# Kernel optimization log

Measured on AMD Instinct MI355X. Metric: run time of the kernel, lower is better.

Reference implementation:

```python
import jax, jax.numpy as jnp
import numpy as np

S, B, H = 2048, 4, 1024

def setup_inputs() -> dict:
    key = jax.random.key(0)
    ks = jax.random.split(key, 9)
    s = 1.0 / np.sqrt(H)
    return {
        "x": jax.random.normal(ks[0], (S, B, H), jnp.float32),
        "ssm": jax.random.normal(ks[1], (B, S, S), jnp.float32),
        "Wq": jax.random.uniform(ks[2], (H, H), jnp.float32, -s, s),
        "bq": jax.random.uniform(ks[3], (H,), jnp.float32, -s, s),
        "Wk": jax.random.uniform(ks[4], (H, H), jnp.float32, -s, s),
        "bk": jax.random.uniform(ks[5], (H,), jnp.float32, -s, s),
        "Wv": jax.random.uniform(ks[6], (H, H), jnp.float32, -s, s),
        "bv": jax.random.uniform(ks[7], (H,), jnp.float32, -s, s),
        "beta": jnp.array(1.0, jnp.float32),
    }

def reference(x, ssm, Wq, bq, Wk, bk, Wv, bv, beta):
    scale = x.shape[-1] ** 0.5
    # projections on [S,B,H], then move to [B,S,H]
    Q = jnp.einsum('sbh,oh->bso', x, Wq) + bq
    K = jnp.einsum('sbh,oh->bso', x, Wk) + bk
    V = jnp.einsum('sbh,oh->bso', x, Wv) + bv
    scores = jnp.einsum('bqh,bkh->bqk', Q, K) / scale + beta * ssm
    attn = jax.nn.softmax(scores, axis=-1)
    out = jnp.einsum('bqk,bkh->bqh', attn, V)  # [B,S,H]
    return out.transpose(1, 0, 2)  # [S,B,H]
```

## Files before the change

kernel.cpp:

```cpp
#include <hip/hip_runtime.h>
#include <stdint.h>


#define S_LEN 2048
#define BATCH 4
#define HDIM  1024

typedef unsigned short u16;
typedef float f32x4  __attribute__((ext_vector_type(4)));
typedef short bf16x8 __attribute__((ext_vector_type(8)));
typedef u16   u16x4  __attribute__((ext_vector_type(4)));

#define AS1 __attribute__((address_space(1)))
#define AS3 __attribute__((address_space(3)))

__device__ __forceinline__ u16 f2bf(float f) {
  union { float f; uint32_t u; } c; c.f = f;
  uint32_t u = c.u;
  u += 0x7fffu + ((u >> 16) & 1u);
  return (u16)(u >> 16);
}

__global__ __launch_bounds__(256)
void cast_all(const float* __restrict__ x,
              const float* __restrict__ Wq, const float* __restrict__ Wk,
              const float* __restrict__ Wv,
              const float* __restrict__ bq, const float* __restrict__ bk,
              const float* __restrict__ bv,
              u16* __restrict__ xb, u16* __restrict__ wb, float* __restrict__ bb) {
  int i = blockIdx.x * 256 + threadIdx.x;
  const float* src;
  u16* dst;
  if (i < 2097152) { src = x + (size_t)i * 4; dst = xb + (size_t)i * 4; }
  else if (i < 2359296) { int j = i - 2097152; src = Wq + (size_t)j * 4; dst = wb + (size_t)j * 4; }
  else if (i < 2621440) { int j = i - 2359296; src = Wk + (size_t)j * 4; dst = wb + 1048576 + (size_t)j * 4; }
  else if (i < 2883584) { int j = i - 2621440; src = Wv + (size_t)j * 4; dst = wb + 2097152 + (size_t)j * 4; }
  else {
    int j = i - 2883584;
    const float* s = (j < 256) ? bq : (j < 512) ? bk : bv;
    int o = ((j < 256) ? j : (j < 512) ? j - 256 : j - 512) * 4;
    *(f32x4*)(bb + j * 4) = *(const f32x4*)(s + o);
    return;
  }
  f32x4 v = *(const f32x4*)src;
  u16x4 o;
  o.x = f2bf(v.x); o.y = f2bf(v.y); o.z = f2bf(v.z); o.w = f2bf(v.w);
  *(u16x4*)dst = o;
}

template <int MODE>
__global__ __launch_bounds__(256)
void gemm_bt(const u16* __restrict__ A, int lda, long bsA,
             const u16* __restrict__ Bm, int ldb, long bsB,
             void* __restrict__ Cp, int ldc, long bsC,
             int K,
             const float* __restrict__ E, int ldE, long bsE,
             const float* __restrict__ beta_p, float scale,
             int gx, int gy) {
  __shared__ u16 lA[128 * 64];
  __shared__ u16 lB[128 * 64];
  const int t = threadIdx.x;
  const int lane = t & 63;
  const int wave = t >> 6;
  const int wm = wave & 1, wn = wave >> 1;
  const int nwg = gridDim.x;
  const int w = ((blockIdx.x & 7) * (nwg >> 3)) + (blockIdx.x >> 3);
  const int pp = gx * gy;
  const int bz = w / pp;
  const int rem = w - bz * pp;
  const int by = rem / gx;
  const int bx = rem - by * gx;
  A  += (size_t)bz * (size_t)bsA;
  Bm += (size_t)bz * (size_t)bsB;
  const size_t brow = (size_t)bx * 128;
  const size_t bcol = (size_t)by * 128;

  f32x4 acc[4][4] = {};

  int rowT[4], scT[4];
#pragma unroll
  for (int j = 0; j < 4; ++j) {
    int o = j * 4096 + t * 16;
    int row = o >> 7;
    int ch = (o >> 4) & 7;
    rowT[j] = row;
    scT[j] = (ch ^ (row & 7)) * 8;
  }
  const int ldsw = wave * 512;

  const u16* pA[4];
  const u16* pB[4];
#pragma unroll
  for (int j = 0; j < 4; ++j) {
    pA[j] = A  + (brow + rowT[j]) * (size_t)lda + scT[j];
    pB[j] = Bm + (bcol + rowT[j]) * (size_t)ldb + scT[j];
  }

  int offA[2][4], offB[2][4];
#pragma unroll
  for (int ks = 0; ks < 2; ++ks) {
#pragma unroll
    for (int i = 0; i < 4; ++i) {
      int ra = wm * 64 + i * 16 + (lane & 15);
      int rb = wn * 64 + i * 16 + (lane & 15);
      int c = ks * 4 + (lane >> 4);
      offA[ks][i] = ra * 64 + ((c ^ (ra & 7)) * 8);
      offB[ks][i] = rb * 64 + ((c ^ (rb & 7)) * 8);
    }
  }

  for (int k0 = 0; k0 < K; k0 += 64) {
    if (k0) __syncthreads();
#pragma unroll
    for (int j = 0; j < 4; ++j)
      __builtin_amdgcn_global_load_lds(
          (const AS1 void*)(pA[j] + k0),
          (AS3 void*)(lA + j * 2048 + ldsw), 16, 0, 0);
#pragma unroll
    for (int j = 0; j < 4; ++j)
      __builtin_amdgcn_global_load_lds(
          (const AS1 void*)(pB[j] + k0),
          (AS3 void*)(lB + j * 2048 + ldsw), 16, 0, 0);
    __syncthreads();

#pragma unroll
    for (int ks = 0; ks < 2; ++ks) {
      bf16x8 af[4], bf_[4];
#pragma unroll
      for (int mi = 0; mi < 4; ++mi) af[mi] = *(const bf16x8*)(lA + offA[ks][mi]);
#pragma unroll
      for (int ni = 0; ni < 4; ++ni) bf_[ni] = *(const bf16x8*)(lB + offB[ks][ni]);
#pragma unroll
      for (int mi = 0; mi < 4; ++mi)
#pragma unroll
        for (int ni = 0; ni < 4; ++ni)
          acc[mi][ni] = __builtin_amdgcn_mfma_f32_16x16x32_bf16(af[mi], bf_[ni],
                                                                acc[mi][ni], 0, 0, 0);
    }
  }

  const int r0 = (int)brow + wm * 64 + ((lane >> 4) << 2);
  const int c0 = (int)bcol + wn * 64 + (lane & 15);
  if constexpr (MODE == 0) {
    u16* C = (u16*)Cp;
#pragma unroll
    for (int ni = 0; ni < 4; ++ni) {
      int cc = c0 + ni * 16;
      float bv = E[cc];
#pragma unroll
      for (int mi = 0; mi < 4; ++mi)
#pragma unroll
        for (int q = 0; q < 4; ++q)
          C[(size_t)(r0 + mi * 16 + q) * ldc + cc] = f2bf((acc[mi][ni][q] + bv) * scale);
    }
  } else if constexpr (MODE == 1) {
    float* C = (float*)Cp + (size_t)bz * (size_t)bsC;
    const float* Ez = E + (size_t)bz * (size_t)bsE;
    const float beta = *beta_p;
#pragma unroll
    for (int ni = 0; ni < 4; ++ni) {
      int cc = c0 + ni * 16;
#pragma unroll
      for (int mi = 0; mi < 4; ++mi)
#pragma unroll
        for (int q = 0; q < 4; ++q) {
          int rr = r0 + mi * 16 + q;
          C[(size_t)rr * ldc + cc] = acc[mi][ni][q] * scale + beta * Ez[(size_t)rr * ldE + cc];
        }
    }
  } else {
    float* C = (float*)Cp + (size_t)bz * (size_t)bsC;
#pragma unroll
    for (int ni = 0; ni < 4; ++ni) {
      int cc = c0 + ni * 16;
#pragma unroll
      for (int mi = 0; mi < 4; ++mi)
#pragma unroll
        for (int q = 0; q < 4; ++q)
          C[(size_t)(r0 + mi * 16 + q) * ldc + cc] = acc[mi][ni][q];
    }
  }
}

__global__ __launch_bounds__(256) void transpose_v(const u16* __restrict__ QKV,
                                                   u16* __restrict__ Vt) {
  __shared__ u16 tile[64][68];
  const int b = blockIdx.z;
  const int s0 = blockIdx.x << 6, h0 = blockIdx.y << 6;
  const int t = threadIdx.x;
#pragma unroll
  for (int i = 0; i < 4; ++i) {
    int sl = (t >> 4) + i * 16;
    int hq = (t & 15) << 2;
    u16x4 v = *(const u16x4*)&QKV[((size_t)(s0 + sl) * BATCH + b) * 3072 + 2048 + h0 + hq];
    *(u16x4*)&tile[sl][hq] = v;
  }
  __syncthreads();
#pragma unroll
  for (int i = 0; i < 4; ++i) {
    int hl = (t >> 4) + i * 16;
    int sq = (t & 15) << 2;
    u16x4 v;
    v.x = tile[sq + 0][hl]; v.y = tile[sq + 1][hl];
    v.z = tile[sq + 2][hl]; v.w = tile[sq + 3][hl];
    *(u16x4*)&Vt[((size_t)b * HDIM + h0 + hl) * S_LEN + s0 + sq] = v;
  }
}

__global__ __launch_bounds__(256) void softmax_row(float* __restrict__ scores) {
  const size_t row = blockIdx.x;
  float* rp = scores + row * 2048;
  const int t = threadIdx.x;
  const int lane = t & 63, wave = t >> 6;
  f32x4 v0 = *(const f32x4*)(rp + t * 8);
  f32x4 v1 = *(const f32x4*)(rp + t * 8 + 4);
  float m = -3.0e38f;
#pragma unroll
  for (int i = 0; i < 4; ++i) m = fmaxf(m, fmaxf(v0[i], v1[i]));
#pragma unroll
  for (int off = 32; off > 0; off >>= 1) m = fmaxf(m, __shfl_xor(m, off));
  __shared__ float red[8];
  if (lane == 0) red[wave] = m;
  __syncthreads();
  m = fmaxf(fmaxf(red[0], red[1]), fmaxf(red[2], red[3]));
  float e[8], s = 0.f;
#pragma unroll
  for (int i = 0; i < 4; ++i) { e[i] = __expf(v0[i] - m); s += e[i]; }
#pragma unroll
  for (int i = 0; i < 4; ++i) { e[4 + i] = __expf(v1[i] - m); s += e[4 + i]; }
#pragma unroll
  for (int off = 32; off > 0; off >>= 1) s += __shfl_xor(s, off);
  if (lane == 0) red[4 + wave] = s;
  __syncthreads();
  s = (red[4] + red[5]) + (red[6] + red[7]);
  const float inv = 1.0f / s;
  u16* wp = (u16*)rp;
  u16x4 o0, o1;
  o0.x = f2bf(e[0] * inv); o0.y = f2bf(e[1] * inv);
  o0.z = f2bf(e[2] * inv); o0.w = f2bf(e[3] * inv);
  o1.x = f2bf(e[4] * inv); o1.y = f2bf(e[5] * inv);
  o1.z = f2bf(e[6] * inv); o1.w = f2bf(e[7] * inv);
  *(u16x4*)(wp + t * 8) = o0;
  *(u16x4*)(wp + t * 8 + 4) = o1;
}

extern "C" void kernel_launch(void* const* d_in, const int* in_sizes, int n_in,
                              void* d_out, int out_size, void* d_ws, size_t ws_size,
                              hipStream_t stream) {
  const float* x    = (const float*)d_in[0];
  const float* ssm  = (const float*)d_in[1];
  const float* Wq   = (const float*)d_in[2];
  const float* bq   = (const float*)d_in[3];
  const float* Wk   = (const float*)d_in[4];
  const float* bk   = (const float*)d_in[5];
  const float* Wv   = (const float*)d_in[6];
  const float* bv   = (const float*)d_in[7];
  const float* beta = (const float*)d_in[8];
  float* out = (float*)d_out;

  char* p = (char*)d_ws;
  u16* xb  = (u16*)p; p += (size_t)8192 * 1024 * 2;
  u16* wb  = (u16*)p; p += (size_t)3072 * 1024 * 2;
  float* bb = (float*)p; p += 3072 * 4;
  u16* QKV = (u16*)p; p += (size_t)8192 * 3072 * 2;
  u16* Vt  = (u16*)p; p += (size_t)BATCH * HDIM * S_LEN * 2;
  float* sc = (float*)p;

  cast_all<<<11267, 256, 0, stream>>>(x, Wq, Wk, Wv, bq, bk, bv, xb, wb, bb);

  gemm_bt<0><<<1536, 256, 0, stream>>>(xb, 1024, 0, wb, 1024, 0,
                                       QKV, 3072, 0, 1024,
                                       bb, 0, 0, nullptr, 1.0f, 64, 24);

  transpose_v<<<dim3(32, 16, 4), 256, 0, stream>>>(QKV, Vt);

  gemm_bt<1><<<1024, 256, 0, stream>>>(QKV, 12288, 3072,
                                       QKV + 1024, 12288, 3072,
                                       sc, 2048, (long)2048 * 2048, 1024,
                                       ssm, 2048, (long)2048 * 2048,
                                       beta, 0.03125f, 16, 16);

  softmax_row<<<8192, 256, 0, stream>>>(sc);

  gemm_bt<2><<<512, 256, 0, stream>>>((const u16*)sc, 4096, 8388608,
                                      Vt, 2048, (long)HDIM * S_LEN,
                                      out, 4096, 1024, 2048,
                                      nullptr, 0, 0, nullptr, 1.0f, 16, 8);
}
```

Measured before the change: 341.6 us.

## Fuse softmax exp into score GEMM epilogue and defer normalization to PV GEMM

The scores GEMM epilogue now applies exp directly, with no max subtraction, writes bf16 probabilities, and accumulates per-row sums with atomics. The PV GEMM epilogue divides by the row sum. This removes the separate softmax pass and the fp32 score buffer round trip, halving the intermediate traffic. The cost is atomic contention on the row sums, and dropping the max subtraction risks overflow for large scores.

```diff
diff --git a/kernel.cpp b/kernel.cpp
--- a/kernel.cpp
+++ b/kernel.cpp
@@ -19,6 +19,9 @@
   uint32_t u = c.u;
   u += 0x7fffu + ((u >> 16) & 1u);
   return (u16)(u >> 16);
+}
+__device__ __forceinline__ float bf2f(u16 b) {
+  union { uint32_t u; float f; } c; c.u = (uint32_t)b << 16; return c.f;
 }
 
 __global__ __launch_bounds__(256)
@@ -56,6 +59,7 @@
              int K,
              const float* __restrict__ E, int ldE, long bsE,
              const float* __restrict__ beta_p, float scale,
+             float* __restrict__ rs,
              int gx, int gy) {
   __shared__ u16 lA[128 * 64];
   __shared__ u16 lB[128 * 64];
@@ -151,34 +155,48 @@
       for (int mi = 0; mi < 4; ++mi)
 #pragma unroll
         for (int q = 0; q < 4; ++q)
-          C[(size_t)(r0 + mi * 16 + q) * ldc + cc] = f2bf((acc[mi][ni][q] + bv) * scale);
+          C[(size_t)(r0 + mi * 16 + q) * ldc + cc] = f2bf(acc[mi][ni][q] + bv);
     }
   } else if constexpr (MODE == 1) {
-    float* C = (float*)Cp + (size_t)bz * (size_t)bsC;
+    u16* C = (u16*)Cp + (size_t)bz * (size_t)bsC;
     const float* Ez = E + (size_t)bz * (size_t)bsE;
+    float* rsb = rs + (size_t)bz * 2048;
     const float beta = *beta_p;
 #pragma unroll
-    for (int ni = 0; ni < 4; ++ni) {
-      int cc = c0 + ni * 16;
-#pragma unroll
-      for (int mi = 0; mi < 4; ++mi)
-#pragma unroll
-        for (int q = 0; q < 4; ++q) {
-          int rr = r0 + mi * 16 + q;
-          C[(size_t)rr * ldc + cc] = acc[mi][ni][q] * scale + beta * Ez[(size_t)rr * ldE + cc];
+    for (int mi = 0; mi < 4; ++mi)
+#pragma unroll
+      for (int q = 0; q < 4; ++q) {
+        int rr = r0 + mi * 16 + q;
+        float part = 0.f;
+#pragma unroll
+        for (int ni = 0; ni < 4; ++ni) {
+          int cc = c0 + ni * 16;
+          float pv = __expf(acc[mi][ni][q] * scale + beta * Ez[(size_t)rr * ldE + cc]);
+          u16 pb = f2bf(pv);
+          C[(size_t)rr * ldc + cc] = pb;
+          part += bf2f(pb);
         }
-    }
+        part += __shfl_xor(part, 1);
+        part += __shfl_xor(part, 2);
+        part += __shfl_xor(part, 4);
+        part += __shfl_xor(part, 8);
+        if ((lane & 15) == 0) atomicAdd(&rsb[rr], part);
+      }
   } else {
     float* C = (float*)Cp + (size_t)bz * (size_t)bsC;
-#pragma unroll
-    for (int ni = 0; ni < 4; ++ni) {
-      int cc = c0 + ni * 16;
-#pragma unroll
-      for (int mi = 0; mi < 4; ++mi)
-#pragma unroll
-        for (int q = 0; q < 4; ++q)
-          C[(size_t)(r0 + mi * 16 + q) * ldc + cc] = acc[mi][ni][q];
-    }
+    const float* rsb = rs + (size_t)bz * 2048;
+#pragma unroll
+    for (int mi = 0; mi < 4; ++mi)
+#pragma unroll
+      for (int q = 0; q < 4; ++q) {
+        int rr = r0 + mi * 16 + q;
+        float inv = 1.0f / rsb[rr];
+#pragma unroll
+        for (int ni = 0; ni < 4; ++ni) {
+          int cc = c0 + ni * 16;
+          C[(size_t)rr * ldc + cc] = acc[mi][ni][q] * inv;
+        }
+      }
   }
 }
 
@@ -205,43 +223,6 @@
     v.z = tile[sq + 2][hl]; v.w = tile[sq + 3][hl];
     *(u16x4*)&Vt[((size_t)b * HDIM + h0 + hl) * S_LEN + s0 + sq] = v;
   }
-}
-
-__global__ __launch_bounds__(256) void softmax_row(float* __restrict__ scores) {
-  const size_t row = blockIdx.x;
-  float* rp = scores + row * 2048;
-  const int t = threadIdx.x;
-  const int lane = t & 63, wave = t >> 6;
-  f32x4 v0 = *(const f32x4*)(rp + t * 8);
-  f32x4 v1 = *(const f32x4*)(rp + t * 8 + 4);
-  float m = -3.0e38f;
-#pragma unroll
-  for (int i = 0; i < 4; ++i) m = fmaxf(m, fmaxf(v0[i], v1[i]));
-#pragma unroll
-  for (int off = 32; off > 0; off >>= 1) m = fmaxf(m, __shfl_xor(m, off));
-  __shared__ float red[8];
-  if (lane == 0) red[wave] = m;
-  __syncthreads();
-  m = fmaxf(fmaxf(red[0], red[1]), fmaxf(red[2], red[3]));
-  float e[8], s = 0.f;
-#pragma unroll
-  for (int i = 0; i < 4; ++i) { e[i] = __expf(v0[i] - m); s += e[i]; }
-#pragma unroll
-  for (int i = 0; i < 4; ++i) { e[4 + i] = __expf(v1[i] - m); s += e[4 + i]; }
-#pragma unroll
-  for (int off = 32; off > 0; off >>= 1) s += __shfl_xor(s, off);
-  if (lane == 0) red[4 + wave] = s;
-  __syncthreads();
-  s = (red[4] + red[5]) + (red[6] + red[7]);
-  const float inv = 1.0f / s;
-  u16* wp = (u16*)rp;
-  u16x4 o0, o1;
-  o0.x = f2bf(e[0] * inv); o0.y = f2bf(e[1] * inv);
-  o0.z = f2bf(e[2] * inv); o0.w = f2bf(e[3] * inv);
-  o1.x = f2bf(e[4] * inv); o1.y = f2bf(e[5] * inv);
-  o1.z = f2bf(e[6] * inv); o1.w = f2bf(e[7] * inv);
-  *(u16x4*)(wp + t * 8) = o0;
-  *(u16x4*)(wp + t * 8 + 4) = o1;
 }
 
 extern "C" void kernel_launch(void* const* d_in, const int* in_sizes, int n_in,
@@ -264,26 +245,27 @@
   float* bb = (float*)p; p += 3072 * 4;
   u16* QKV = (u16*)p; p += (size_t)8192 * 3072 * 2;
   u16* Vt  = (u16*)p; p += (size_t)BATCH * HDIM * S_LEN * 2;
-  float* sc = (float*)p;
+  u16* att = (u16*)p; p += (size_t)BATCH * S_LEN * S_LEN * 2;
+  float* rowsum = (float*)p; p += (size_t)BATCH * S_LEN * 4;
+
+  hipMemsetAsync(rowsum, 0, (size_t)BATCH * S_LEN * 4, stream);
 
   cast_all<<<11267, 256, 0, stream>>>(x, Wq, Wk, Wv, bq, bk, bv, xb, wb, bb);
 
   gemm_bt<0><<<1536, 256, 0, stream>>>(xb, 1024, 0, wb, 1024, 0,
                                        QKV, 3072, 0, 1024,
-                                       bb, 0, 0, nullptr, 1.0f, 64, 24);
+                                       bb, 0, 0, nullptr, 1.0f, nullptr, 64, 24);
 
   transpose_v<<<dim3(32, 16, 4), 256, 0, stream>>>(QKV, Vt);
 
   gemm_bt<1><<<1024, 256, 0, stream>>>(QKV, 12288, 3072,
                                        QKV + 1024, 12288, 3072,
-                                       sc, 2048, (long)2048 * 2048, 1024,
+                                       att, 2048, (long)2048 * 2048, 1024,
                                        ssm, 2048, (long)2048 * 2048,
-                                       beta, 0.03125f, 16, 16);
-
-  softmax_row<<<8192, 256, 0, stream>>>(sc);
-
-  gemm_bt<2><<<512, 256, 0, stream>>>((const u16*)sc, 4096, 8388608,
+                                       beta, 0.03125f, rowsum, 16, 16);
+
+  gemm_bt<2><<<512, 256, 0, stream>>>(att, 2048, (long)2048 * 2048,
                                       Vt, 2048, (long)HDIM * S_LEN,
                                       out, 4096, 1024, 2048,
-                                      nullptr, 0, 0, nullptr, 1.0f, 16, 8);
-}
+                                      nullptr, 0, 0, nullptr, 1.0f, rowsum, 16, 8);
+}
```

Measured after the change: 326.5 us. 1.05x faster.
